# Performance work log

Hardware: AMD Instinct MI355X
Metric: run time of the kernel (lower is better)

The kernel has to match this reference:

```python
import jax, jax.numpy as jnp
import numpy as np

EPS = 1e-6  # T5LayerNorm epsilon


def setup_inputs() -> dict:
    key = jax.random.key(0)
    k0, k1, k2, k3 = jax.random.split(key, 4)
    B, S, D, F, E = 4, 2048, 768, 3072, 8
    hidden_states = jax.random.normal(k0, (B, S, D), jnp.float32)
    router_w = jax.random.normal(k1, (E, D), jnp.float32) * 0.02
    ln_w = jnp.ones((E, D), jnp.float32)
    wi = jax.random.normal(k2, (E, F, D), jnp.float32) * 0.02
    wo = jax.random.normal(k3, (E, D, F), jnp.float32) * 0.02
    return {"hidden_states": hidden_states, "router_w": router_w, "ln_w": ln_w,
            "wi": wi, "wo": wo, "top_k": 2}


def reference(hidden_states, router_w, ln_w, wi, wo, top_k):
    B, S, D = hidden_states.shape
    E = router_w.shape[0]
    x = hidden_states.reshape(-1, D)                      # [T, D] tokens
    router_logits = x @ router_w.T                        # [T, E]
    probs = jax.nn.softmax(router_logits, axis=-1)
    rw, sel = jax.lax.top_k(probs, top_k)                 # [T, K]
    rw = rw / jnp.sum(rw, axis=-1, keepdims=True)         # renormalize top-k weights

    # T5LayerNorm is RMS-norm (no mean subtraction); shared input x, per-expert scale.
    var = jnp.mean(x * x, axis=-1, keepdims=True)         # [T, 1]
    x_norm = x * jax.lax.rsqrt(var + EPS)                 # [T, D]

    out = jnp.zeros_like(x)
    for e in range(E):  # fixed small loop over experts (structurally distinct params)
        # combine weight for expert e: zero for tokens that did not select it
        w_e = jnp.sum(jnp.where(sel == e, rw, 0.0), axis=-1)   # [T]
        h = x_norm * ln_w[e]                                   # [T, D]
        ff = jax.nn.relu(h @ wi[e].T) @ wo[e].T                # [T, D]
        # T5LayerFF returns x + FFN(LN(x)); routing weight scales the whole output
        out = out + w_e[:, None] * (x + ff)
    layer_output = out.reshape(B, S, D)
    return layer_output, router_logits
```

## Files before the change

### kernel.cpp

```cpp
#include <hip/hip_runtime.h>
#include <hip/hip_bf16.h>
#include <math.h>

typedef short short8 __attribute__((ext_vector_type(8)));
typedef float f32x16 __attribute__((ext_vector_type(16)));

constexpr int D = 768;
constexpr int E = 8;
constexpr int F = 3072;
constexpr int T = 8192;
constexpr float EPS = 1e-6f;

static __device__ inline unsigned short f2bf(float f) {
    __hip_bfloat16 h = __float2bfloat16(f);
    return *reinterpret_cast<unsigned short*>(&h);
}

static __device__ inline f32x16 mfma_bf16(short8 a, short8 b, f32x16 c) {
    return __builtin_amdgcn_mfma_f32_32x32x16_bf16(a, b, c, 0, 0, 0);
}

#define GLL16(g, s) __builtin_amdgcn_global_load_lds( \
    (const __attribute__((address_space(1))) unsigned int*)(g), \
    (__attribute__((address_space(3))) unsigned int*)(s), 16, 0, 0)

__global__ __launch_bounds__(256)
void prep_kernel(const float* __restrict__ wi, const float* __restrict__ wo,
                 const float* __restrict__ lnw,
                 unsigned short* __restrict__ wip, unsigned short* __restrict__ wop,
                 const float* __restrict__ x, const float* __restrict__ rw,
                 float* __restrict__ logits, unsigned short* __restrict__ xn,
                 float* __restrict__ out, int* __restrict__ sel,
                 float2* __restrict__ w01)
{
    if (blockIdx.x < 36864) {
        const unsigned NWI = (unsigned)E * F * D;
        unsigned i4 = (blockIdx.x * 256u + threadIdx.x) * 4u;
        if (i4 < NWI) {
            float4 v = *(const float4*)(wi + i4);
            unsigned e = i4 / (unsigned)(F * D);
            unsigned d = i4 % (unsigned)D;
            float4 l = *(const float4*)(lnw + e * D + d);
            ushort4 o = { f2bf(v.x * l.x), f2bf(v.y * l.y), f2bf(v.z * l.z), f2bf(v.w * l.w) };
            *(ushort4*)(wip + i4) = o;
        } else {
            unsigned j = i4 - NWI;
            float4 v = *(const float4*)(wo + j);
            ushort4 o = { f2bf(v.x), f2bf(v.y), f2bf(v.z), f2bf(v.w) };
            *(ushort4*)(wop + j) = o;
        }
        return;
    }

    const int lane = threadIdx.x & 63;
    const int wid  = threadIdx.x >> 6;
    const int t = (blockIdx.x - 36864) * 4 + wid;
    if (t >= T) return;

    const float* xr = x + (size_t)t * D;
    float xv[12];
    float acc[8];
#pragma unroll
    for (int e = 0; e < 8; ++e) acc[e] = 0.f;
    float ssq = 0.f;
#pragma unroll
    for (int i = 0; i < 12; ++i) {
        const int k = lane + 64 * i;
        const float v = xr[k];
        xv[i] = v;
        ssq += v * v;
#pragma unroll
        for (int e = 0; e < 8; ++e) acc[e] += v * rw[e * D + k];
    }
#pragma unroll
    for (int off = 32; off; off >>= 1) {
        ssq += __shfl_xor(ssq, off);
#pragma unroll
        for (int e = 0; e < 8; ++e) acc[e] += __shfl_xor(acc[e], off);
    }

    int e0 = 0; float m0 = acc[0];
#pragma unroll
    for (int e = 1; e < 8; ++e) if (acc[e] > m0) { m0 = acc[e]; e0 = e; }
    int e1 = -1; float m1 = -3.4e38f;
#pragma unroll
    for (int e = 0; e < 8; ++e) if (e != e0 && acc[e] > m1) { m1 = acc[e]; e1 = e; }

    const float r  = expf(m1 - m0);
    const float w0 = 1.f / (1.f + r);
    const float w1 = r * w0;
    const float wsum = w0 + w1;
    const float rs = rsqrtf(ssq * (1.f / (float)D) + EPS);

    if (lane == 0) {
#pragma unroll
        for (int e = 0; e < 8; ++e) logits[t * 8 + e] = acc[e];
        sel[t] = e0 | (e1 << 4);
        w01[t] = make_float2(w0, w1);
    }

#pragma unroll
    for (int i = 0; i < 12; ++i) {
        const int k = lane + 64 * i;
        xn[(size_t)t * D + k] = f2bf(xv[i] * rs);
        out[(size_t)t * D + k] = wsum * xv[i];
    }
}

__global__ __launch_bounds__(256)
void lists_kernel(const int* __restrict__ sel, const float2* __restrict__ w01,
                  int* __restrict__ offs,
                  int* __restrict__ lists, float* __restrict__ wlist)
{
    const int e = blockIdx.x;
    const int tid = threadIdx.x;
    const int lane = tid & 63;
    const int wv = tid >> 6;

    __shared__ int sc[4][8];
    __shared__ int wtot[4];

    int c[8];
#pragma unroll
    for (int i = 0; i < 8; ++i) c[i] = 0;
    for (int t = tid; t < T; t += 256) {
        const int s = sel[t];
        const int a = s & 15, b = (s >> 4) & 15;
#pragma unroll
        for (int i = 0; i < 8; ++i) c[i] += (a == i) + (b == i);
    }
#pragma unroll
    for (int off = 32; off; off >>= 1)
#pragma unroll
        for (int i = 0; i < 8; ++i) c[i] += __shfl_xor(c[i], off);
    if (lane == 0)
#pragma unroll
        for (int i = 0; i < 8; ++i) sc[wv][i] = c[i];
    __syncthreads();

    int cnt8[8];
#pragma unroll
    for (int i = 0; i < 8; ++i) cnt8[i] = sc[0][i] + sc[1][i] + sc[2][i] + sc[3][i];
    int base = 0;
#pragma unroll
    for (int i = 0; i < 8; ++i) if (i < e) base += cnt8[i];

    if (e == 0 && tid == 0) {
        int a = 0;
#pragma unroll
        for (int i = 0; i < 8; ++i) { offs[i] = a; a += cnt8[i]; }
        offs[8] = a;
    }

    int cnt = 0;
    for (int c0 = 0; c0 < T; c0 += 256) {
        const int t = c0 + tid;
        const int s = sel[t];
        const bool m1 = ((s >> 4) & 15) == e;
        const bool m = ((s & 15) == e) || m1;
        const unsigned long long b = __ballot(m);
        const int pre = __popcll(b & ((1ULL << lane) - 1ULL));
        if (lane == 0) wtot[wv] = __popcll(b);
        __syncthreads();
        int wbase = 0;
#pragma unroll
        for (int i = 0; i < 4; ++i) if (i < wv) wbase += wtot[i];
        if (m) {
            const int pos = base + cnt + wbase + pre;
            lists[pos] = (t << 1) | (m1 ? 1 : 0);
            const float2 w = w01[t];
            wlist[pos] = m1 ? w.y : w.x;
        }
        cnt += wtot[0] + wtot[1] + wtot[2] + wtot[3];
        __syncthreads();
    }
}


__global__ __launch_bounds__(256)
void gemm1_kernel(const unsigned short* __restrict__ xn,
                  const unsigned short* __restrict__ wip,
                  const int* __restrict__ offs,
                  const int* __restrict__ lists,
                  unsigned short* __restrict__ H)
{
    __shared__ unsigned short sA[128 * 64];
    __shared__ unsigned short sB[128 * 64];
    __shared__ int s_tok[128];

    const int bid = blockIdx.x;
    const int e  = bid & 7;
    const int q  = bid >> 3;
    const int mt = q / 24;
    const int nt = q % 24;
    const int offe = offs[e];
    const int cnt = offs[e + 1] - offe;
    const int base = mt * 128;
    if (base >= cnt) return;

    const int tid = threadIdx.x;
    const int w = tid >> 6, l = tid & 63;
    const int lo = l & 31, hi = l >> 5;
    const int wr = w >> 1, wc = w & 1;

    if (tid < 128) {
        const int idx = base + tid;
        s_tok[tid] = (idx < cnt) ? (lists[offe + idx] >> 1) : 0;
    }
    __syncthreads();

    const int r = (w * 4 + 0) * 8 + (l >> 3);
    const int chS = ((l & 7) ^ ((l >> 3) & 7)) * 8;
    const unsigned short* aSrc[4];
    const unsigned short* bSrc[4];
#pragma unroll
    for (int j = 0; j < 4; ++j) {
        const int rj = r + j * 8;
        aSrc[j] = xn + (size_t)s_tok[rj] * D + chS;
        bSrc[j] = wip + ((size_t)e * F + nt * 128 + rj) * D + chS;
    }
    char* sAc = (char*)sA;
    char* sBc = (char*)sB;

    f32x16 acc00, acc01, acc10, acc11;
#pragma unroll
    for (int qq = 0; qq < 16; ++qq) { acc00[qq] = 0.f; acc01[qq] = 0.f; acc10[qq] = 0.f; acc11[qq] = 0.f; }

    const int rx = (lo & 7) << 4;
    const int arow0 = (wr * 64 + lo) * 128;
    const int arow1 = arow0 + 32 * 128;
    const int brow0 = (wc * 64 + lo) * 128;
    const int brow1 = brow0 + 32 * 128;

    for (int kt = 0; kt < 12; ++kt) {
        const int k0 = kt * 64;
#pragma unroll
        for (int j = 0; j < 4; ++j) {
            GLL16(aSrc[j] + k0, sAc + (w * 4 + j) * 1024);
            GLL16(bSrc[j] + k0, sBc + (w * 4 + j) * 1024);
        }
        __syncthreads();
#pragma unroll
        for (int ks = 0; ks < 4; ++ks) {
            const int coff = (hi * 16 + ks * 32) ^ rx;
            short8 a0 = *(const short8*)(sAc + arow0 + coff);
            short8 a1 = *(const short8*)(sAc + arow1 + coff);
            short8 b0 = *(const short8*)(sBc + brow0 + coff);
            short8 b1 = *(const short8*)(sBc + brow1 + coff);
            acc00 = mfma_bf16(a0, b0, acc00);
            acc01 = mfma_bf16(a0, b1, acc01);
            acc10 = mfma_bf16(a1, b0, acc10);
            acc11 = mfma_bf16(a1, b1, acc11);
        }
        __syncthreads();
    }

    const int cbase = nt * 128 + wc * 64 + lo;
#pragma unroll
    for (int rr = 0; rr < 16; ++rr) {
        const int crow = (rr & 3) + 8 * (rr >> 2) + 4 * hi;
        int lrow = wr * 64 + crow;
        if (base + lrow < cnt) {
            unsigned short* hp = H + (size_t)(offe + base + lrow) * F + cbase;
            hp[0]  = f2bf(fmaxf(acc00[rr], 0.f));
            hp[32] = f2bf(fmaxf(acc01[rr], 0.f));
        }
        lrow += 32;
        if (base + lrow < cnt) {
            unsigned short* hp = H + (size_t)(offe + base + lrow) * F + cbase;
            hp[0]  = f2bf(fmaxf(acc10[rr], 0.f));
            hp[32] = f2bf(fmaxf(acc11[rr], 0.f));
        }
    }
}

__global__ __launch_bounds__(256)
void gemm2_kernel(const unsigned short* __restrict__ H,
                  const unsigned short* __restrict__ wop,
                  const int* __restrict__ offs,
                  const int* __restrict__ lists, const float* __restrict__ wlist,
                  float* __restrict__ ffout0, float* __restrict__ ffout1,
                  int kts)
{
    __shared__ unsigned short sA[128 * 64];
    __shared__ unsigned short sB[128 * 64];
    __shared__ int   s_tok[128];
    __shared__ float s_wgt[128];

    const int bid = blockIdx.x;
    const int e  = bid & 7;
    const int q  = bid >> 3;
    const int kh = q / 384;
    const int rm = q % 384;
    const int mt = rm / 6;
    const int nt = rm % 6;
    const int offe = offs[e];
    const int cnt = offs[e + 1] - offe;
    const int base = mt * 128;
    if (base >= cnt) return;

    const int tid = threadIdx.x;
    const int w = tid >> 6, l = tid & 63;
    const int lo = l & 31, hi = l >> 5;
    const int wr = w >> 1, wc = w & 1;

    if (tid < 128) {
        const int idx = base + tid;
        const bool v = idx < cnt;
        s_tok[tid] = v ? lists[offe + idx] : 0;
        s_wgt[tid] = v ? wlist[offe + idx] : 0.f;
    }
    __syncthreads();

    const int kof = kh * kts * 64;
    const int r = (w * 4 + 0) * 8 + (l >> 3);
    const int chS = ((l & 7) ^ ((l >> 3) & 7)) * 8;
    const unsigned short* aSrc[4];
    const unsigned short* bSrc[4];
#pragma unroll
    for (int j = 0; j < 4; ++j) {
        const int rj = r + j * 8;
        aSrc[j] = H + (size_t)(offe + base + rj) * F + kof + chS;
        bSrc[j] = wop + ((size_t)e * D + nt * 128 + rj) * F + kof + chS;
    }
    char* sAc = (char*)sA;
    char* sBc = (char*)sB;

    f32x16 acc00, acc01, acc10, acc11;
#pragma unroll
    for (int qq = 0; qq < 16; ++qq) { acc00[qq] = 0.f; acc01[qq] = 0.f; acc10[qq] = 0.f; acc11[qq] = 0.f; }

    const int rx = (lo & 7) << 4;
    const int arow0 = (wr * 64 + lo) * 128;
    const int arow1 = arow0 + 32 * 128;
    const int brow0 = (wc * 64 + lo) * 128;
    const int brow1 = brow0 + 32 * 128;

    for (int kt = 0; kt < kts; ++kt) {
        const int k0 = kt * 64;
#pragma unroll
        for (int j = 0; j < 4; ++j) {
            GLL16(aSrc[j] + k0, sAc + (w * 4 + j) * 1024);
            GLL16(bSrc[j] + k0, sBc + (w * 4 + j) * 1024);
        }
        __syncthreads();
#pragma unroll
        for (int ks = 0; ks < 4; ++ks) {
            const int coff = (hi * 16 + ks * 32) ^ rx;
            short8 a0 = *(const short8*)(sAc + arow0 + coff);
            short8 a1 = *(const short8*)(sAc + arow1 + coff);
            short8 b0 = *(const short8*)(sBc + brow0 + coff);
            short8 b1 = *(const short8*)(sBc + brow1 + coff);
            acc00 = mfma_bf16(a0, b0, acc00);
            acc01 = mfma_bf16(a0, b1, acc01);
            acc10 = mfma_bf16(a1, b0, acc10);
            acc11 = mfma_bf16(a1, b1, acc11);
        }
        __syncthreads();
    }

    float* fbase = kh ? ffout1 : ffout0;
    const int cbase = nt * 128 + wc * 64 + lo;
#pragma unroll
    for (int rr = 0; rr < 16; ++rr) {
        const int crow = (rr & 3) + 8 * (rr >> 2) + 4 * hi;
#pragma unroll
        for (int mh = 0; mh < 2; ++mh) {
            const int lrow = wr * 64 + crow + mh * 32;
            if (base + lrow < cnt) {
                const int pk = s_tok[lrow];
                const float wgt = s_wgt[lrow];
                float* dst = fbase + ((size_t)(pk & 1) * T + (pk >> 1)) * D + cbase;
                dst[0]  = wgt * (mh ? acc10[rr] : acc00[rr]);
                dst[32] = wgt * (mh ? acc11[rr] : acc01[rr]);
            }
        }
    }
}

__global__ __launch_bounds__(256)
void combine_kernel(const float* __restrict__ f0, const float* __restrict__ f1,
                    int nkh, float* __restrict__ out)
{
    const long long i4 = ((long long)blockIdx.x * 256 + threadIdx.x) * 4;
    float4 o  = *(const float4*)(out + i4);
    float4 a0 = *(const float4*)(f0 + i4);
    float4 a1 = *(const float4*)(f0 + (long long)T * D + i4);
    o.x += a0.x + a1.x; o.y += a0.y + a1.y;
    o.z += a0.z + a1.z; o.w += a0.w + a1.w;
    if (nkh == 2) {
        float4 b0 = *(const float4*)(f1 + i4);
        float4 b1 = *(const float4*)(f1 + (long long)T * D + i4);
        o.x += b0.x + b1.x; o.y += b0.y + b1.y;
        o.z += b0.z + b1.z; o.w += b0.w + b1.w;
    }
    *(float4*)(out + i4) = o;
}

extern "C" void kernel_launch(void* const* d_in, const int* in_sizes, int n_in,
                              void* d_out, int out_size, void* d_ws, size_t ws_size,
                              hipStream_t stream) {
    const float* x   = (const float*)d_in[0];
    const float* rw  = (const float*)d_in[1];
    const float* lnw = (const float*)d_in[2];
    const float* wi  = (const float*)d_in[3];
    const float* wo  = (const float*)d_in[4];

    float* out    = (float*)d_out;
    float* logits = (float*)d_out + (size_t)T * D;

    char* ws = (char*)d_ws;
    unsigned short* xn     = (unsigned short*)(ws);
    unsigned short* wip    = (unsigned short*)(ws + 12582912);
    float*          ffout0 = (float*)(ws);
    unsigned short* wop    = (unsigned short*)(ws + 50331648);
    unsigned short* H      = (unsigned short*)(ws + 88080384);
    int*            offs   = (int*)(ws + 190316544);
    int*            sel    = (int*)(ws + 190316672);
    float2*         w01    = (float2*)(ws + 190349440);
    int*            lists  = (int*)(ws + 190414976);
    float*          wlist  = (float*)(ws + 190480512);
    float*          ffout1 = (float*)(ws + 190578688);

    const bool big2 = ws_size >= 240910336ULL;
    const int nkh = big2 ? 2 : 1;
    const int kts = 48 / nkh;

    prep_kernel<<<36864 + T / 4, 256, 0, stream>>>(wi, wo, lnw, wip, wop,
                                                   x, rw, logits, xn, out,
                                                   sel, w01);

    lists_kernel<<<E, 256, 0, stream>>>(sel, w01, offs, lists, wlist);

    gemm1_kernel<<<64 * 24 * 8, 256, 0, stream>>>(xn, wip, offs, lists, H);
    gemm2_kernel<<<nkh * 64 * 6 * 8, 256, 0, stream>>>(H, wop, offs, lists,
                                                       wlist, ffout0,
                                                       big2 ? ffout1 : ffout0,
                                                       kts);
    combine_kernel<<<T * D / 4 / 256, 256, 0, stream>>>(ffout0,
                                                        big2 ? ffout1 : ffout0,
                                                        nkh, out);
}
```

Before: 333.4 us.

## Widen gemm2 tile to 128x256 with 512 threads; fold residual into combine

gemm2 now uses 512-thread blocks with a 128x256 output tile, so the A tile (H rows) is loaded once and reused across twice as many output columns. A and B share one 48KB LDS buffer. The residual term wsum*x is no longer written by prep_kernel and then read back in combine. combine now reads x and the routing weights and computes it directly, removing one full fp32 write and read of the output. In exchange, the larger LDS footprint and block size may lower occupancy, and the grid of gemm2 blocks is halved.

```diff
diff --git a/kernel.cpp b/kernel.cpp
--- a/kernel.cpp
+++ b/kernel.cpp
@@ -30,8 +30,7 @@
                  unsigned short* __restrict__ wip, unsigned short* __restrict__ wop,
                  const float* __restrict__ x, const float* __restrict__ rw,
                  float* __restrict__ logits, unsigned short* __restrict__ xn,
-                 float* __restrict__ out, int* __restrict__ sel,
-                 float2* __restrict__ w01)
+                 int* __restrict__ sel, float2* __restrict__ w01)
 {
     if (blockIdx.x < 36864) {
         const unsigned NWI = (unsigned)E * F * D;
@@ -89,7 +88,6 @@
     const float r  = expf(m1 - m0);
     const float w0 = 1.f / (1.f + r);
     const float w1 = r * w0;
-    const float wsum = w0 + w1;
     const float rs = rsqrtf(ssq * (1.f / (float)D) + EPS);
 
     if (lane == 0) {
@@ -103,7 +101,6 @@
     for (int i = 0; i < 12; ++i) {
         const int k = lane + 64 * i;
         xn[(size_t)t * D + k] = f2bf(xv[i] * rs);
-        out[(size_t)t * D + k] = wsum * xv[i];
     }
 }
 
@@ -175,7 +172,6 @@
         __syncthreads();
     }
 }
-
 
 __global__ __launch_bounds__(256)
 void gemm1_kernel(const unsigned short* __restrict__ xn,
@@ -274,7 +270,7 @@
     }
 }
 
-__global__ __launch_bounds__(256)
+__global__ __launch_bounds__(512)
 void gemm2_kernel(const unsigned short* __restrict__ H,
                   const unsigned short* __restrict__ wop,
                   const int* __restrict__ offs,
@@ -282,18 +278,17 @@
                   float* __restrict__ ffout0, float* __restrict__ ffout1,
                   int kts)
 {
-    __shared__ unsigned short sA[128 * 64];
-    __shared__ unsigned short sB[128 * 64];
+    __shared__ unsigned short sT[384 * 64];
     __shared__ int   s_tok[128];
     __shared__ float s_wgt[128];
 
     const int bid = blockIdx.x;
     const int e  = bid & 7;
     const int q  = bid >> 3;
-    const int kh = q / 384;
-    const int rm = q % 384;
-    const int mt = rm / 6;
-    const int nt = rm % 6;
+    const int kh = q / 192;
+    const int rm = q % 192;
+    const int mt = rm / 3;
+    const int nt = rm % 3;
     const int offe = offs[e];
     const int cnt = offs[e + 1] - offe;
     const int base = mt * 128;
@@ -302,7 +297,8 @@
     const int tid = threadIdx.x;
     const int w = tid >> 6, l = tid & 63;
     const int lo = l & 31, hi = l >> 5;
-    const int wr = w >> 1, wc = w & 1;
+    const int wr = w >> 2;
+    const int wcn = w & 3;
 
     if (tid < 128) {
         const int idx = base + tid;
@@ -313,18 +309,20 @@
     __syncthreads();
 
     const int kof = kh * kts * 64;
-    const int r = (w * 4 + 0) * 8 + (l >> 3);
-    const int chS = ((l & 7) ^ ((l >> 3) & 7)) * 8;
-    const unsigned short* aSrc[4];
-    const unsigned short* bSrc[4];
-#pragma unroll
-    for (int j = 0; j < 4; ++j) {
-        const int rj = r + j * 8;
-        aSrc[j] = H + (size_t)(offe + base + rj) * F + kof + chS;
-        bSrc[j] = wop + ((size_t)e * D + nt * 128 + rj) * F + kof + chS;
-    }
-    char* sAc = (char*)sA;
-    char* sBc = (char*)sB;
+    const int srow = tid >> 3;
+    const int chS = ((tid & 7) ^ (srow & 7)) * 8;
+    const unsigned short* src6[6];
+#pragma unroll
+    for (int c = 0; c < 6; ++c) {
+        const int rrow = srow + c * 64;
+        if (rrow < 128) {
+            src6[c] = H + (size_t)(offe + base + rrow) * F + kof + chS;
+        } else {
+            src6[c] = wop + ((size_t)e * D + nt * 256 + (rrow - 128)) * F + kof + chS;
+        }
+    }
+    char* sTc = (char*)sT;
+    const int dOff = srow * 128 + (tid & 7) * 16;
 
     f32x16 acc00, acc01, acc10, acc11;
 #pragma unroll
@@ -333,24 +331,22 @@
     const int rx = (lo & 7) << 4;
     const int arow0 = (wr * 64 + lo) * 128;
     const int arow1 = arow0 + 32 * 128;
-    const int brow0 = (wc * 64 + lo) * 128;
+    const int brow0 = (128 + wcn * 64 + lo) * 128;
     const int brow1 = brow0 + 32 * 128;
 
     for (int kt = 0; kt < kts; ++kt) {
         const int k0 = kt * 64;
 #pragma unroll
-        for (int j = 0; j < 4; ++j) {
-            GLL16(aSrc[j] + k0, sAc + (w * 4 + j) * 1024);
-            GLL16(bSrc[j] + k0, sBc + (w * 4 + j) * 1024);
-        }
+        for (int c = 0; c < 6; ++c)
+            GLL16(src6[c] + k0, sTc + c * 8192 + dOff);
         __syncthreads();
 #pragma unroll
         for (int ks = 0; ks < 4; ++ks) {
             const int coff = (hi * 16 + ks * 32) ^ rx;
-            short8 a0 = *(const short8*)(sAc + arow0 + coff);
-            short8 a1 = *(const short8*)(sAc + arow1 + coff);
-            short8 b0 = *(const short8*)(sBc + brow0 + coff);
-            short8 b1 = *(const short8*)(sBc + brow1 + coff);
+            short8 a0 = *(const short8*)(sTc + arow0 + coff);
+            short8 a1 = *(const short8*)(sTc + arow1 + coff);
+            short8 b0 = *(const short8*)(sTc + brow0 + coff);
+            short8 b1 = *(const short8*)(sTc + brow1 + coff);
             acc00 = mfma_bf16(a0, b0, acc00);
             acc01 = mfma_bf16(a0, b1, acc01);
             acc10 = mfma_bf16(a1, b0, acc10);
@@ -360,7 +356,7 @@
     }
 
     float* fbase = kh ? ffout1 : ffout0;
-    const int cbase = nt * 128 + wc * 64 + lo;
+    const int cbase = nt * 256 + wcn * 64 + lo;
 #pragma unroll
     for (int rr = 0; rr < 16; ++rr) {
         const int crow = (rr & 3) + 8 * (rr >> 2) + 4 * hi;
@@ -379,15 +375,19 @@
 }
 
 __global__ __launch_bounds__(256)
-void combine_kernel(const float* __restrict__ f0, const float* __restrict__ f1,
+void combine_kernel(const float* __restrict__ x, const float2* __restrict__ w01,
+                    const float* __restrict__ f0, const float* __restrict__ f1,
                     int nkh, float* __restrict__ out)
 {
     const long long i4 = ((long long)blockIdx.x * 256 + threadIdx.x) * 4;
-    float4 o  = *(const float4*)(out + i4);
+    const int t = (int)(i4 / D);
+    const float2 wp = w01[t];
+    const float ws = wp.x + wp.y;
+    float4 xv = *(const float4*)(x + i4);
     float4 a0 = *(const float4*)(f0 + i4);
     float4 a1 = *(const float4*)(f0 + (long long)T * D + i4);
-    o.x += a0.x + a1.x; o.y += a0.y + a1.y;
-    o.z += a0.z + a1.z; o.w += a0.w + a1.w;
+    float4 o = { ws * xv.x + a0.x + a1.x, ws * xv.y + a0.y + a1.y,
+                 ws * xv.z + a0.z + a1.z, ws * xv.w + a0.w + a1.w };
     if (nkh == 2) {
         float4 b0 = *(const float4*)(f1 + i4);
         float4 b1 = *(const float4*)(f1 + (long long)T * D + i4);
@@ -427,17 +427,17 @@
     const int kts = 48 / nkh;
 
     prep_kernel<<<36864 + T / 4, 256, 0, stream>>>(wi, wo, lnw, wip, wop,
-                                                   x, rw, logits, xn, out,
+                                                   x, rw, logits, xn,
                                                    sel, w01);
 
     lists_kernel<<<E, 256, 0, stream>>>(sel, w01, offs, lists, wlist);
 
     gemm1_kernel<<<64 * 24 * 8, 256, 0, stream>>>(xn, wip, offs, lists, H);
-    gemm2_kernel<<<nkh * 64 * 6 * 8, 256, 0, stream>>>(H, wop, offs, lists,
+    gemm2_kernel<<<nkh * 64 * 3 * 8, 512, 0, stream>>>(H, wop, offs, lists,
                                                        wlist, ffout0,
                                                        big2 ? ffout1 : ffout0,
                                                        kts);
-    combine_kernel<<<T * D / 4 / 256, 256, 0, stream>>>(ffout0,
+    combine_kernel<<<T * D / 4 / 256, 256, 0, stream>>>(x, w01, ffout0,
                                                         big2 ? ffout1 : ffout0,
                                                         nkh, out);
 }
```

New measurement: 316.9 us (median of 2 runs). 1.05x faster.
